# Kernel tuning notes

Hardware: AMD Instinct MI355X
Metric: run time of the kernel (lower is better)

## Reference

```python
import jax, jax.numpy as jnp
import numpy as np

B, T, DIN, P, HID, L = 256, 512, 25, 128, 256, 5
Q = 0.15
EPS = 1e-5


def setup_inputs() -> dict:
    key = jax.random.key(0)
    ks = jax.random.split(key, 12)
    s = 0.05
    return {
        "x": jax.random.normal(ks[0], (B, T, DIN), jnp.float32),
        "lengths": jax.random.randint(ks[1], (B,), 1, T + 1),
        "ln_g": jnp.ones((DIN,), jnp.float32),
        "ln_b": jnp.zeros((DIN,), jnp.float32),
        "w1": jax.random.normal(ks[2], (DIN, P), jnp.float32) * s,
        "b1": jnp.zeros((P,), jnp.float32),
        "w2": jax.random.normal(ks[3], (P, P), jnp.float32) * s,
        "b2": jnp.zeros((P,), jnp.float32),
        "Wih0": jax.random.normal(ks[4], (2, 3 * HID, P), jnp.float32) * s,
        "Whh0": jax.random.normal(ks[5], (2, 3 * HID, HID), jnp.float32) * s,
        "bih0": jnp.zeros((2, 3 * HID), jnp.float32),
        "bhh0": jnp.zeros((2, 3 * HID), jnp.float32),
        "Wih": jax.random.normal(ks[6], (L - 1, 2, 3 * HID, 2 * HID), jnp.float32) * s,
        "Whh": jax.random.normal(ks[7], (L - 1, 2, 3 * HID, HID), jnp.float32) * s,
        "bih": jnp.zeros((L - 1, 2, 3 * HID), jnp.float32),
        "bhh": jnp.zeros((L - 1, 2, 3 * HID), jnp.float32),
        "Wc": jax.random.normal(ks[8], (2 * HID,), jnp.float32) * s,
        "bc": jnp.zeros((), jnp.float32),
    }


def _gru_dir(xs, mask, Wih, Whh, bih, bhh):
    """Masked unidirectional GRU (PyTorch gate convention). xs:[B,T,Din], mask:[B,T] -> [B,T,HID]."""
    xw = jnp.einsum('btd,gd->btg', xs, Wih) + bih  # [B,T,3H] precomputed input gates

    def step(h, inp):
        xw_t, m_t = inp  # [B,3H], [B]
        gh = h @ Whh.T + bhh
        r = jax.nn.sigmoid(xw_t[:, :HID] + gh[:, :HID])
        z = jax.nn.sigmoid(xw_t[:, HID:2 * HID] + gh[:, HID:2 * HID])
        n = jnp.tanh(xw_t[:, 2 * HID:] + r * gh[:, 2 * HID:])
        h_new = (1.0 - z) * n + z * h
        h = jnp.where(m_t[:, None], h_new, h)        # hold state past sequence end (packing)
        return h, jnp.where(m_t[:, None], h, 0.0)    # padded outputs are zero (pad_packed)

    h0 = jnp.zeros((xs.shape[0], HID), xs.dtype)
    _, ys = jax.lax.scan(step, h0, (xw.transpose(1, 0, 2), mask.T))
    return ys.transpose(1, 0, 2)


def reference(x, lengths, ln_g, ln_b, w1, b1, w2, b2,
              Wih0, Whh0, bih0, bhh0, Wih, Whh, bih, bhh, Wc, bc):
    mask = jnp.arange(T)[None, :] < lengths[:, None]  # [B,T]

    # InputProjection: LayerNorm -> Linear -> GELU(exact) -> Linear
    mu = x.mean(-1, keepdims=True)
    var = ((x - mu) ** 2).mean(-1, keepdims=True)
    xn = (x - mu) / jnp.sqrt(var + EPS) * ln_g + ln_b
    h = jax.nn.gelu(xn @ w1 + b1, approximate=False) @ w2 + b2  # [B,T,P]

    # per-sample time reversal indices (reverse valid prefix only)
    rev = jnp.clip(lengths[:, None] - 1 - jnp.arange(T)[None, :], 0, T - 1)  # [B,T]

    inp = h
    for l in range(L):
        Wi = Wih0 if l == 0 else Wih[l - 1]
        Wh = Whh0 if l == 0 else Whh[l - 1]
        bi = bih0 if l == 0 else bih[l - 1]
        bh = bhh0 if l == 0 else bhh[l - 1]
        yf = _gru_dir(inp, mask, Wi[0], Wh[0], bi[0], bh[0])
        x_rev = jnp.take_along_axis(inp, rev[:, :, None], axis=1) * mask[:, :, None]
        yb_rev = _gru_dir(x_rev, mask, Wi[1], Wh[1], bi[1], bh[1])
        yb = jnp.take_along_axis(yb_rev, rev[:, :, None], axis=1) * mask[:, :, None]
        inp = jnp.concatenate([yf, yb], axis=-1)  # [B,T,2H]
    H = inp

    # TopQPooling: per-sample variable-k top-k by L2-norm score, then mean
    scores = jnp.where(mask, jnp.linalg.norm(H, axis=2), -1e9)
    k_vals = jnp.maximum(jnp.ceil(lengths.astype(jnp.float32) * Q).astype(jnp.int32), 1)  # [B]
    order = jnp.argsort(-scores, axis=1)                      # descending by score
    topmask = jnp.arange(T)[None, :] < k_vals[:, None]        # first k of sorted order
    Hs = jnp.take_along_axis(H, order[:, :, None], axis=1)
    pooled = (Hs * topmask[:, :, None]).sum(axis=1) / k_vals[:, None].astype(H.dtype)

    logits = pooled @ Wc + bc  # [B]
    return logits
```

## Files before the change

kernel.cpp:

```cpp
#include <hip/hip_runtime.h>
#include <math.h>


#define CH 64

__global__ __launch_bounds__(256)
void sort_k(const int* __restrict__ len, int* __restrict__ perm,
            int* __restrict__ nchp, int Bg)
{
    __shared__ int ll[256];
    __shared__ int lp[256];
    const int i = threadIdx.x;
    const int li = len[i];
    ll[i] = li;
    __syncthreads();
    int rk = 0;
    for (int j = 0; j < 256; j++) {
        int lj = ll[j];
        rk += (lj < li || (lj == li && j < i)) ? 1 : 0;
    }
    lp[rk] = i;
    __syncthreads();
    perm[i] = lp[i];
    const int ngrp = 256 / Bg;
    if (i < ngrp) {
        int mx = ll[lp[i * Bg + Bg - 1]];
        int nch = (mx + 63) >> 6;
        nchp[i] = nch < 1 ? 1 : (nch > 8 ? 8 : nch);
    }
}

__global__ __launch_bounds__(256)
void prep_whhT_k(const float* __restrict__ Whh0, const float* __restrict__ Whh,
                 float* __restrict__ out)
{
    int id = blockIdx.x * 256 + threadIdx.x;
    int u = id / 196608, rr = id % 196608;
    int k = rr / 768, c = rr % 768;
    int l = u >> 1, d = u & 1;
    out[id] = (l == 0) ? Whh0[(size_t)(d * 768 + c) * 256 + k]
                       : Whh[(size_t)(((l - 1) * 2 + d) * 768 + c) * 256 + k];
}

__global__ __launch_bounds__(128)
void input_proj_k(const float* __restrict__ x, const int* __restrict__ lengths,
                  const int* __restrict__ perm,
                  const float* __restrict__ lng, const float* __restrict__ lnb,
                  const float* __restrict__ w1, const float* __restrict__ b1v,
                  const float* __restrict__ w2, const float* __restrict__ b2v,
                  float* __restrict__ out, int g0)
{
    const int btl = blockIdx.x;
    const int sl  = btl >> 9;
    const int t   = btl & 511;
    const int b   = perm[g0 + sl];
    if (t >= lengths[b]) return;
    const int tid = threadIdx.x;
    __shared__ float xs[25];
    __shared__ float xn[25];
    __shared__ float hs[128];
    if (tid < 25) xs[tid] = x[((size_t)b * 512 + t) * 25 + tid];
    __syncthreads();
    if (tid < 25) {
        float mu = 0.f;
        #pragma unroll
        for (int k = 0; k < 25; k++) mu += xs[k];
        mu *= (1.f / 25.f);
        float var = 0.f;
        #pragma unroll
        for (int k = 0; k < 25; k++) { float dd = xs[k] - mu; var += dd * dd; }
        var *= (1.f / 25.f);
        float rstd = 1.f / sqrtf(var + 1e-5f);
        xn[tid] = (xs[tid] - mu) * rstd * lng[tid] + lnb[tid];
    }
    __syncthreads();
    float a = b1v[tid];
    #pragma unroll
    for (int k = 0; k < 25; k++) a = fmaf(xn[k], w1[k * 128 + tid], a);
    float ge = 0.5f * a * (1.f + erff(a * 0.70710678118654752440f));
    hs[tid] = ge;
    __syncthreads();
    float o = b2v[tid];
    #pragma unroll 8
    for (int k = 0; k < 128; k++) o = fmaf(hs[k], w2[k * 128 + tid], o);
    out[(size_t)btl * 128 + tid] = o;
}

__global__ __launch_bounds__(256)
void round_k(const float* __restrict__ A, int K,
             const float* __restrict__ W,
             const float* __restrict__ bi,
             const int* __restrict__ lengths, const int* __restrict__ perm,
             const int* __restrict__ nchp, int gidx, int g0, int Bg,
             float* __restrict__ xw_w,
             const float* __restrict__ xw_r,
             const float* __restrict__ whhT,
             const float* __restrict__ bhh,
             float* __restrict__ Y,
             float* __restrict__ hstate,
             int NR, int r)
{
    __shared__ float As[8][68];
    __shared__ float Bs[8][132];
    __shared__ float h_s[260];
    __shared__ float gs[4][776];

    const int tid = threadIdx.x;
    const int nch = nchp[gidx];

    if ((int)blockIdx.x < NR) {
        if (r == 0) return;
        const int d   = ((int)blockIdx.x >= Bg) ? 1 : 0;
        const int s   = (int)blockIdx.x - d * Bg;
        const int lo  = d ? (nch - r) * 64 : (r - 1) * 64;
        if (lo < 0 || lo >= 512) return;
        const int len = lengths[perm[g0 + s]];
        int nst = min(lo + CH, len) - lo;
        if (nst < 0) nst = 0;
        const int first = (r == 1);
        if (!first && nst <= 0) return;

        float* hg = hstate + (size_t)(d * Bg + s) * 256;
        h_s[tid] = first ? 0.f : hg[tid];
        __syncthreads();

        const int kq  = tid >> 6;
        const int q4  = (tid & 63) * 4;
        const float* Wd  = whhT + (size_t)d * 196608;
        const float* xwd = xw_r + (size_t)(d * Bg + s) * 64 * 768;
        const float bh0 = bhh[d * 768 + tid];
        const float bh1 = bhh[d * 768 + 256 + tid];
        const float bh2 = bhh[d * 768 + 512 + tid];

        for (int st = 0; st < nst; st++) {
            const int p = d ? (lo + nst - 1 - st) : (lo + st);
            float a0[4] = {}, a1[4] = {}, a2[4] = {};
            const float* wk = Wd + (size_t)(kq * 64) * 768 + q4;
            #pragma unroll 4
            for (int k4 = 0; k4 < 16; k4++) {
                float4 h4 = *(const float4*)&h_s[kq * 64 + k4 * 4];
                const float* w0 = wk + (size_t)(k4 * 4) * 768;
                float hk[4] = {h4.x, h4.y, h4.z, h4.w};
                #pragma unroll
                for (int kk = 0; kk < 4; kk++) {
                    const float* wr = w0 + (size_t)kk * 768;
                    float4 wv0 = *(const float4*)(wr);
                    float4 wv1 = *(const float4*)(wr + 256);
                    float4 wv2 = *(const float4*)(wr + 512);
                    float h = hk[kk];
                    a0[0] = fmaf(h, wv0.x, a0[0]); a0[1] = fmaf(h, wv0.y, a0[1]);
                    a0[2] = fmaf(h, wv0.z, a0[2]); a0[3] = fmaf(h, wv0.w, a0[3]);
                    a1[0] = fmaf(h, wv1.x, a1[0]); a1[1] = fmaf(h, wv1.y, a1[1]);
                    a1[2] = fmaf(h, wv1.z, a1[2]); a1[3] = fmaf(h, wv1.w, a1[3]);
                    a2[0] = fmaf(h, wv2.x, a2[0]); a2[1] = fmaf(h, wv2.y, a2[1]);
                    a2[2] = fmaf(h, wv2.z, a2[2]); a2[3] = fmaf(h, wv2.w, a2[3]);
                }
            }
            *(float4*)&gs[kq][q4]       = make_float4(a0[0], a0[1], a0[2], a0[3]);
            *(float4*)&gs[kq][256 + q4] = make_float4(a1[0], a1[1], a1[2], a1[3]);
            *(float4*)&gs[kq][512 + q4] = make_float4(a2[0], a2[1], a2[2], a2[3]);
            __syncthreads();
            float gr = bh0 + gs[0][tid] + gs[1][tid] + gs[2][tid] + gs[3][tid];
            float gz = bh1 + gs[0][256 + tid] + gs[1][256 + tid]
                           + gs[2][256 + tid] + gs[3][256 + tid];
            float gn = bh2 + gs[0][512 + tid] + gs[1][512 + tid]
                           + gs[2][512 + tid] + gs[3][512 + tid];
            const float* xr = xwd + (size_t)(p - lo) * 768;
            float rg = 1.f / (1.f + expf(-(xr[tid] + gr)));
            float zg = 1.f / (1.f + expf(-(xr[256 + tid] + gz)));
            float ng = tanhf(xr[512 + tid] + rg * gn);
            float hv = h_s[tid];
            float hn = (1.f - zg) * ng + zg * hv;
            h_s[tid] = hn;
            Y[((size_t)(s * 512 + p)) * 512 + d * 256 + tid] = hn;
            __syncthreads();
        }
        hg[tid] = h_s[tid];
    } else {
        const int gid  = blockIdx.x - NR;
        const int nt   = gid % 6;
        const int rest = gid / 6;
        const int d    = (rest >= Bg) ? 1 : 0;
        const int s    = rest - d * Bg;
        const int lo   = d ? (nch - 1 - r) * 64 : r * 64;
        if (lo < 0 || lo >= 512) return;
        if (lengths[perm[g0 + s]] <= lo) return;

        float acc[4][8] = {};
        const int tm = tid >> 4;
        const int tn = tid & 15;
        const int arr = tid >> 2, ak = (tid & 3) * 2;
        const int bn = tid >> 1, bk = (tid & 1) * 4;

        const float* Ap = A + (size_t)(s * 512 + lo + arr) * K + ak;
        const float* Wp = W + ((size_t)d * 768 + nt * 128 + bn) * K + bk;

        for (int k0 = 0; k0 < K; k0 += 8) {
            float2 av = *(const float2*)(Ap + k0);
            float4 bv = *(const float4*)(Wp + k0);
            __syncthreads();
            As[ak][arr] = av.x; As[ak + 1][arr] = av.y;
            Bs[bk + 0][bn] = bv.x; Bs[bk + 1][bn] = bv.y;
            Bs[bk + 2][bn] = bv.z; Bs[bk + 3][bn] = bv.w;
            __syncthreads();
            #pragma unroll
            for (int kk = 0; kk < 8; kk++) {
                float4 a4 = *(const float4*)&As[kk][tm * 4];
                float4 b0v = *(const float4*)&Bs[kk][tn * 4];
                float4 b1v = *(const float4*)&Bs[kk][64 + tn * 4];
                float ar4[4] = {a4.x, a4.y, a4.z, a4.w};
                float br[8] = {b0v.x, b0v.y, b0v.z, b0v.w,
                               b1v.x, b1v.y, b1v.z, b1v.w};
                #pragma unroll
                for (int i = 0; i < 4; i++)
                    #pragma unroll
                    for (int j = 0; j < 8; j++)
                        acc[i][j] = fmaf(ar4[i], br[j], acc[i][j]);
            }
        }
        const int cb = d * 768 + nt * 128;
        float bv0[4], bv1[4];
        #pragma unroll
        for (int j = 0; j < 4; j++) {
            bv0[j] = bi[cb + tn * 4 + j];
            bv1[j] = bi[cb + 64 + tn * 4 + j];
        }
        #pragma unroll
        for (int i = 0; i < 4; i++) {
            const int row = tm * 4 + i;
            float* o = xw_w + (size_t)((d * Bg + s) * 64 + row) * 768 + nt * 128 + tn * 4;
            float4 c0 = make_float4(acc[i][0] + bv0[0], acc[i][1] + bv0[1],
                                    acc[i][2] + bv0[2], acc[i][3] + bv0[3]);
            float4 c1 = make_float4(acc[i][4] + bv1[0], acc[i][5] + bv1[1],
                                    acc[i][6] + bv1[2], acc[i][7] + bv1[3]);
            *(float4*)(o)      = c0;
            *(float4*)(o + 64) = c1;
        }
    }
}

__global__ __launch_bounds__(256)
void pool_k(const float* __restrict__ H, const int* __restrict__ lengths,
            const int* __restrict__ perm,
            const float* __restrict__ Wc, const float* __restrict__ bcp,
            float* __restrict__ out, int g0)
{
    const int bl = blockIdx.x;
    const int b  = perm[g0 + bl];
    const int tid = threadIdx.x;
    __shared__ float sc[512];
    __shared__ int   sel[128];
    __shared__ int   nsel;
    __shared__ float red[256];
    const int len = lengths[b];
    const int k = max(1, (int)ceilf((float)len * 0.15f));
    if (tid == 0) nsel = 0;
    for (int t = tid; t < 512; t += 256) {
        float s;
        if (t < len) {
            const float* row = H + ((size_t)bl * 512 + t) * 512;
            float acc = 0.f;
            for (int j = 0; j < 512; j++) acc = fmaf(row[j], row[j], acc);
            s = sqrtf(acc);
        } else s = -1e9f;
        sc[t] = s;
    }
    __syncthreads();
    for (int t = tid; t < 512; t += 256) {
        if (t < len) {
            const float s = sc[t];
            int cnt = 0;
            for (int u = 0; u < 512; u++) {
                float su = sc[u];
                cnt += (su > s || (su == s && u < t)) ? 1 : 0;
            }
            if (cnt < k) { int p = atomicAdd(&nsel, 1); sel[p] = t; }
        }
    }
    __syncthreads();
    const int ns = nsel;
    float part = 0.f;
    for (int j = tid; j < 512; j += 256) {
        float acc = 0.f;
        for (int i = 0; i < ns; i++)
            acc += H[((size_t)bl * 512 + sel[i]) * 512 + j];
        part += (acc / (float)k) * Wc[j];
    }
    red[tid] = part;
    __syncthreads();
    for (int s2 = 128; s2 > 0; s2 >>= 1) {
        if (tid < s2) red[tid] += red[tid + s2];
        __syncthreads();
    }
    if (tid == 0) out[b] = red[0] + bcp[0];
}

static inline size_t alup(size_t x) { return (x + 255) & ~255ull; }

static size_t tier_bytes(int Bg)
{
    return 2 * alup((size_t)Bg * 512 * 512 * 4)
         + 2 * alup((size_t)Bg * 2 * 64 * 768 * 4)
         + alup(1966080ull * 4)
         + alup((size_t)Bg * 2 * 256 * 4)
         + alup(2048);
}

extern "C" void kernel_launch(void* const* d_in, const int* in_sizes, int n_in,
                              void* d_out, int out_size, void* d_ws, size_t ws_size,
                              hipStream_t stream)
{
    const float* x    = (const float*)d_in[0];
    const int*   len  = (const int*)  d_in[1];
    const float* ln_g = (const float*)d_in[2];
    const float* ln_b = (const float*)d_in[3];
    const float* w1   = (const float*)d_in[4];
    const float* b1   = (const float*)d_in[5];
    const float* w2   = (const float*)d_in[6];
    const float* b2   = (const float*)d_in[7];
    const float* Wih0 = (const float*)d_in[8];
    const float* Whh0 = (const float*)d_in[9];
    const float* bih0 = (const float*)d_in[10];
    const float* bhh0 = (const float*)d_in[11];
    const float* Wih  = (const float*)d_in[12];
    const float* Whh  = (const float*)d_in[13];
    const float* bih  = (const float*)d_in[14];
    const float* bhh  = (const float*)d_in[15];
    const float* Wc   = (const float*)d_in[16];
    const float* bc   = (const float*)d_in[17];
    float* out = (float*)d_out;

    int Bg = 0;
    const int tiers[5] = {128, 64, 32, 16, 8};
    for (int i = 0; i < 5; i++)
        if (ws_size >= tier_bytes(tiers[i])) { Bg = tiers[i]; break; }
    if (Bg == 0) return;

    char* ws = (char*)d_ws;
    size_t off = 0;
    auto alloc = [&](size_t bytes) { size_t o = off; off += alup(bytes); return o; };
    float* h0    = (float*)(ws + alloc((size_t)Bg * 512 * 512 * 4));
    float* h1    = (float*)(ws + alloc((size_t)Bg * 512 * 512 * 4));
    float* xwA   = (float*)(ws + alloc((size_t)Bg * 2 * 64 * 768 * 4));
    float* xwB   = (float*)(ws + alloc((size_t)Bg * 2 * 64 * 768 * 4));
    float* whhT  = (float*)(ws + alloc(1966080ull * 4));
    float* hst   = (float*)(ws + alloc((size_t)Bg * 2 * 256 * 4));
    int*   perm  = (int*)  (ws + alloc(2048));
    int*   nchp  = perm + 256;
    float* xwbuf[2] = {xwA, xwB};

    sort_k<<<1, 256, 0, stream>>>(len, perm, nchp, Bg);
    prep_whhT_k<<<7680, 256, 0, stream>>>(Whh0, Whh, whhT);

    const int NR = 2 * Bg;
    const int NG = 12 * Bg;

    for (int g0 = 0; g0 < 256; g0 += Bg) {
        const int gidx = g0 / Bg;
        input_proj_k<<<Bg * 512, 128, 0, stream>>>(x, len, perm, ln_g, ln_b,
                                                   w1, b1, w2, b2, h0, g0);
        float* bin = h0;
        float* bout = h1;
        for (int l = 0; l < 5; l++) {
            const int K = (l == 0) ? 128 : 512;
            const float* Wl  = (l == 0) ? Wih0 : (Wih + (size_t)(l - 1) * 2 * 768 * 512);
            const float* bil = (l == 0) ? bih0 : (bih + (size_t)(l - 1) * 1536);
            const float* whl = whhT + (size_t)l * 393216;
            const float* bhl = (l == 0) ? bhh0 : (bhh + (size_t)(l - 1) * 1536);
            for (int r = 0; r <= 8; r++) {
                round_k<<<NR + NG, 256, 0, stream>>>(
                    bin, K, Wl, bil, len, perm, nchp, gidx, g0, Bg,
                    xwbuf[r & 1], xwbuf[(r & 1) ^ 1],
                    whl, bhl, bout, hst, NR, r);
            }
            float* tmp = bin; bin = bout; bout = tmp;
        }
        pool_k<<<Bg, 256, 0, stream>>>(bin, len, perm, Wc, bc, out, g0);
    }
}
```

Measured before the change: 48.07 ms.

## Split GRU recurrence across 8-block groups with register-resident weights and flag sync

The recurrent part of each round is reorganised so that every block handles a 32-column slice of the hidden state for a group of 8 sequences, rather than one block computing the full 256-wide state of a single sequence. Each block keeps its slice of the recurrent weights in registers, so the Whh matrix is no longer re-streamed from memory at every timestep. After each step the blocks exchange hidden-state slices through a double-buffered global array, signalled with per-step release/acquire flags stamped with an epoch number. This spreads the serial matvec across more CUs and removes the repeated weight reads. In exchange it adds inter-block spin-waiting, relies on all 8 blocks of a group being co-resident to avoid deadlock, and processes padded steps up to the longest length in each group.

```diff
diff --git a/kernel.cpp b/kernel.cpp
--- a/kernel.cpp
+++ b/kernel.cpp
@@ -3,6 +3,11 @@
 
 
 #define CH 64
+
+#define AT_LOAD_RLX(p)    __hip_atomic_load((p),  __ATOMIC_RELAXED, __HIP_MEMORY_SCOPE_AGENT)
+#define AT_LOAD_ACQ(p)    __hip_atomic_load((p),  __ATOMIC_ACQUIRE, __HIP_MEMORY_SCOPE_AGENT)
+#define AT_STORE_RLX(p,v) __hip_atomic_store((p),(v),__ATOMIC_RELAXED, __HIP_MEMORY_SCOPE_AGENT)
+#define AT_STORE_REL(p,v) __hip_atomic_store((p),(v),__ATOMIC_RELEASE, __HIP_MEMORY_SCOPE_AGENT)
 
 __global__ __launch_bounds__(256)
 void sort_k(const int* __restrict__ len, int* __restrict__ perm,
@@ -97,13 +102,14 @@
              const float* __restrict__ whhT,
              const float* __restrict__ bhh,
              float* __restrict__ Y,
-             float* __restrict__ hstate,
-             int NR, int r)
+             int* __restrict__ hx,
+             int* __restrict__ flags,
+             int NR, int r, int epoch)
 {
     __shared__ float As[8][68];
     __shared__ float Bs[8][132];
-    __shared__ float h_s[260];
-    __shared__ float gs[4][776];
+    __shared__ float hsh[8][256];
+    __shared__ float gsb[8][8][96];
 
     const int tid = threadIdx.x;
     const int nch = nchp[gidx];
@@ -111,71 +117,124 @@
     if ((int)blockIdx.x < NR) {
         if (r == 0) return;
         const int d   = ((int)blockIdx.x >= Bg) ? 1 : 0;
-        const int s   = (int)blockIdx.x - d * Bg;
-        const int lo  = d ? (nch - r) * 64 : (r - 1) * 64;
+        const int rr2 = (int)blockIdx.x - d * Bg;
+        const int sg  = rr2 >> 3;
+        const int sl  = rr2 & 7;
+        const int lo  = d ? (nch - r) * CH : (r - 1) * CH;
         if (lo < 0 || lo >= 512) return;
-        const int len = lengths[perm[g0 + s]];
-        int nst = min(lo + CH, len) - lo;
-        if (nst < 0) nst = 0;
-        const int first = (r == 1);
-        if (!first && nst <= 0) return;
-
-        float* hg = hstate + (size_t)(d * Bg + s) * 256;
-        h_s[tid] = first ? 0.f : hg[tid];
+        const int mlsg = lengths[perm[g0 + sg * 8 + 7]];
+        int nst = min(lo + CH, mlsg) - lo;
+        if (nst <= 0) return;
+        const bool first = d ? (mlsg <= lo + CH) : (r == 1);
+
+        const int kq = tid >> 5;
+        const int jj = tid & 31;
+
+        const float* wb = whhT + (size_t)d * 196608 + (size_t)(kq * 32) * 768
+                        + sl * 32 + jj;
+        float w0[32], w1[32], w2[32];
+        #pragma unroll
+        for (int k = 0; k < 32; k++) {
+            const float* wr = wb + (size_t)k * 768;
+            w0[k] = wr[0];
+            w1[k] = wr[256];
+            w2[k] = wr[512];
+        }
+
+        const int s2 = tid >> 5;
+        const int j2 = tid & 31;
+        const int lens2 = lengths[perm[g0 + sg * 8 + s2]];
+        const float bh0 = bhh[d * 768 +       sl * 32 + j2];
+        const float bh1 = bhh[d * 768 + 256 + sl * 32 + j2];
+        const float bh2 = bhh[d * 768 + 512 + sl * 32 + j2];
+        const int sgN = Bg >> 3;
+        int* flg = flags + (size_t)((d * sgN + sg) * 8) * 64;
+        const int PS  = 2 * Bg * 256;
+        const int hxq = (d * Bg + sg * 8) * 256;
+        float* hf = &hsh[0][0];
+
+        if (first) {
+            #pragma unroll
+            for (int i = 0; i < 8; i++) hf[tid * 8 + i] = 0.f;
+        } else {
+            const int pprev = d ? (lo + nst) : (lo - 1);
+            const int par0  = pprev & 1;
+            #pragma unroll
+            for (int i = 0; i < 8; i++) {
+                const int m = tid * 8 + i;
+                hf[m] = __int_as_float(AT_LOAD_RLX(&hx[par0 * PS + hxq + m]));
+            }
+        }
         __syncthreads();
 
-        const int kq  = tid >> 6;
-        const int q4  = (tid & 63) * 4;
-        const float* Wd  = whhT + (size_t)d * 196608;
-        const float* xwd = xw_r + (size_t)(d * Bg + s) * 64 * 768;
-        const float bh0 = bhh[d * 768 + tid];
-        const float bh1 = bhh[d * 768 + 256 + tid];
-        const float bh2 = bhh[d * 768 + 512 + tid];
+        const float* xwd = xw_r + (size_t)(d * Bg + sg * 8) * 64 * 768 + sl * 32 + j2;
+        const int m0   = tid * 8;
+        const int dim0 = m0 & 255;
+        int* fpoll = &flg[(dim0 >> 5) * 64];
 
         for (int st = 0; st < nst; st++) {
-            const int p = d ? (lo + nst - 1 - st) : (lo + st);
-            float a0[4] = {}, a1[4] = {}, a2[4] = {};
-            const float* wk = Wd + (size_t)(kq * 64) * 768 + q4;
-            #pragma unroll 4
-            for (int k4 = 0; k4 < 16; k4++) {
-                float4 h4 = *(const float4*)&h_s[kq * 64 + k4 * 4];
-                const float* w0 = wk + (size_t)(k4 * 4) * 768;
-                float hk[4] = {h4.x, h4.y, h4.z, h4.w};
+            const int p   = d ? (lo + nst - 1 - st) : (lo + st);
+            const int row = p - lo;
+            const float* xr = xwd + (size_t)(s2 * 64 + row) * 768;
+            const float xv0 = xr[0], xv1 = xr[256], xv2 = xr[512];
+
+            #pragma unroll
+            for (int s = 0; s < 8; s++) {
+                float b0 = 0.f, b1 = 0.f, b2 = 0.f;
                 #pragma unroll
-                for (int kk = 0; kk < 4; kk++) {
-                    const float* wr = w0 + (size_t)kk * 768;
-                    float4 wv0 = *(const float4*)(wr);
-                    float4 wv1 = *(const float4*)(wr + 256);
-                    float4 wv2 = *(const float4*)(wr + 512);
-                    float h = hk[kk];
-                    a0[0] = fmaf(h, wv0.x, a0[0]); a0[1] = fmaf(h, wv0.y, a0[1]);
-                    a0[2] = fmaf(h, wv0.z, a0[2]); a0[3] = fmaf(h, wv0.w, a0[3]);
-                    a1[0] = fmaf(h, wv1.x, a1[0]); a1[1] = fmaf(h, wv1.y, a1[1]);
-                    a1[2] = fmaf(h, wv1.z, a1[2]); a1[3] = fmaf(h, wv1.w, a1[3]);
-                    a2[0] = fmaf(h, wv2.x, a2[0]); a2[1] = fmaf(h, wv2.y, a2[1]);
-                    a2[2] = fmaf(h, wv2.z, a2[2]); a2[3] = fmaf(h, wv2.w, a2[3]);
+                for (int k4 = 0; k4 < 8; k4++) {
+                    const float4 h4 = *(const float4*)&hsh[s][kq * 32 + k4 * 4];
+                    b0 = fmaf(h4.x, w0[k4 * 4 + 0], b0);
+                    b0 = fmaf(h4.y, w0[k4 * 4 + 1], b0);
+                    b0 = fmaf(h4.z, w0[k4 * 4 + 2], b0);
+                    b0 = fmaf(h4.w, w0[k4 * 4 + 3], b0);
+                    b1 = fmaf(h4.x, w1[k4 * 4 + 0], b1);
+                    b1 = fmaf(h4.y, w1[k4 * 4 + 1], b1);
+                    b1 = fmaf(h4.z, w1[k4 * 4 + 2], b1);
+                    b1 = fmaf(h4.w, w1[k4 * 4 + 3], b1);
+                    b2 = fmaf(h4.x, w2[k4 * 4 + 0], b2);
+                    b2 = fmaf(h4.y, w2[k4 * 4 + 1], b2);
+                    b2 = fmaf(h4.z, w2[k4 * 4 + 2], b2);
+                    b2 = fmaf(h4.w, w2[k4 * 4 + 3], b2);
                 }
-            }
-            *(float4*)&gs[kq][q4]       = make_float4(a0[0], a0[1], a0[2], a0[3]);
-            *(float4*)&gs[kq][256 + q4] = make_float4(a1[0], a1[1], a1[2], a1[3]);
-            *(float4*)&gs[kq][512 + q4] = make_float4(a2[0], a2[1], a2[2], a2[3]);
+                gsb[kq][s][jj]      = b0;
+                gsb[kq][s][32 + jj] = b1;
+                gsb[kq][s][64 + jj] = b2;
+            }
             __syncthreads();
-            float gr = bh0 + gs[0][tid] + gs[1][tid] + gs[2][tid] + gs[3][tid];
-            float gz = bh1 + gs[0][256 + tid] + gs[1][256 + tid]
-                           + gs[2][256 + tid] + gs[3][256 + tid];
-            float gn = bh2 + gs[0][512 + tid] + gs[1][512 + tid]
-                           + gs[2][512 + tid] + gs[3][512 + tid];
-            const float* xr = xwd + (size_t)(p - lo) * 768;
-            float rg = 1.f / (1.f + expf(-(xr[tid] + gr)));
-            float zg = 1.f / (1.f + expf(-(xr[256 + tid] + gz)));
-            float ng = tanhf(xr[512 + tid] + rg * gn);
-            float hv = h_s[tid];
+
+            float gr = bh0, gz = bh1, gn = bh2;
+            #pragma unroll
+            for (int q = 0; q < 8; q++) {
+                gr += gsb[q][s2][j2];
+                gz += gsb[q][s2][32 + j2];
+                gn += gsb[q][s2][64 + j2];
+            }
+            const float rg = 1.f / (1.f + expf(-(xv0 + gr)));
+            const float zg = 1.f / (1.f + expf(-(xv1 + gz)));
+            const float ng = tanhf(xv2 + rg * gn);
+            const float hv = hsh[s2][sl * 32 + j2];
             float hn = (1.f - zg) * ng + zg * hv;
-            h_s[tid] = hn;
-            Y[((size_t)(s * 512 + p)) * 512 + d * 256 + tid] = hn;
+            if (p >= lens2) hn = hv;
+            const int par = p & 1;
+            AT_STORE_RLX(&hx[par * PS + hxq + s2 * 256 + sl * 32 + j2],
+                         __float_as_int(hn));
+            if (p < lens2)
+                Y[((size_t)((sg * 8 + s2) * 512 + p)) * 512 + d * 256 + sl * 32 + j2] = hn;
             __syncthreads();
-        }
-        hg[tid] = h_s[tid];
+
+            if (st == nst - 1) break;
+            if (tid == 0) AT_STORE_REL(&flg[sl * 64 + st], epoch);
+            {
+                int* f = fpoll + st;
+                while (AT_LOAD_ACQ(f) != epoch) __builtin_amdgcn_s_sleep(2);
+                #pragma unroll
+                for (int i = 0; i < 8; i++)
+                    hf[m0 + i] = __int_as_float(
+                        AT_LOAD_RLX(&hx[par * PS + hxq + m0 + i]));
+            }
+            __syncthreads();
+        }
     } else {
         const int gid  = blockIdx.x - NR;
         const int nt   = gid % 6;
@@ -302,7 +361,8 @@
     return 2 * alup((size_t)Bg * 512 * 512 * 4)
          + 2 * alup((size_t)Bg * 2 * 64 * 768 * 4)
          + alup(1966080ull * 4)
-         + alup((size_t)Bg * 2 * 256 * 4)
+         + alup((size_t)4 * Bg * 256 * 4)
+         + alup((size_t)2 * (Bg / 8) * 8 * 64 * 4)
          + alup(2048);
 }
 
@@ -344,10 +404,14 @@
     float* xwA   = (float*)(ws + alloc((size_t)Bg * 2 * 64 * 768 * 4));
     float* xwB   = (float*)(ws + alloc((size_t)Bg * 2 * 64 * 768 * 4));
     float* whhT  = (float*)(ws + alloc(1966080ull * 4));
-    float* hst   = (float*)(ws + alloc((size_t)Bg * 2 * 256 * 4));
+    int*   hx    = (int*)  (ws + alloc((size_t)4 * Bg * 256 * 4));
+    const size_t flagBytes = (size_t)2 * (Bg / 8) * 8 * 64 * 4;
+    int*   flags = (int*)  (ws + alloc(flagBytes));
     int*   perm  = (int*)  (ws + alloc(2048));
     int*   nchp  = perm + 256;
     float* xwbuf[2] = {xwA, xwB};
+
+    hipMemsetAsync(flags, 0, flagBytes, stream);
 
     sort_k<<<1, 256, 0, stream>>>(len, perm, nchp, Bg);
     prep_whhT_k<<<7680, 256, 0, stream>>>(Whh0, Whh, whhT);
@@ -368,10 +432,11 @@
             const float* whl = whhT + (size_t)l * 393216;
             const float* bhl = (l == 0) ? bhh0 : (bhh + (size_t)(l - 1) * 1536);
             for (int r = 0; r <= 8; r++) {
+                const int ep = (gidx * 5 + l) * 9 + r + 1;
                 round_k<<<NR + NG, 256, 0, stream>>>(
                     bin, K, Wl, bil, len, perm, nchp, gidx, g0, Bg,
                     xwbuf[r & 1], xwbuf[(r & 1) ^ 1],
-                    whl, bhl, bout, hst, NR, r);
+                    whl, bhl, bout, hx, flags, NR, r, ep);
             }
             float* tmp = bin; bin = bout; bout = tmp;
         }
```

After: 78.57 ms. 63.4% more time.

## Batch eight sequences per recurrent block to reuse Whh loads across samples

Applied to the files above, without the earlier changes.

The recurrent GRU blocks now each process eight length-sorted sequences together instead of one. Each thread owns one hidden unit across all three gates and reads Whh once per step, reusing it for eight hidden states. This replaces the split-K shared-memory reduction, removes one barrier per step, and double-buffers h. The Whh transpose layout changes to match, padded steps are masked per sample, and a Bg=256 workspace tier is added. The trade-off is fewer recurrent blocks (NR = Bg/4), so less parallelism on the serial critical path, with more registers per thread.

```diff
diff --git a/kernel.cpp b/kernel.cpp
--- a/kernel.cpp
+++ b/kernel.cpp
@@ -35,11 +35,15 @@
                  float* __restrict__ out)
 {
     int id = blockIdx.x * 256 + threadIdx.x;
-    int u = id / 196608, rr = id % 196608;
-    int k = rr / 768, c = rr % 768;
-    int l = u >> 1, d = u & 1;
-    out[id] = (l == 0) ? Whh0[(size_t)(d * 768 + c) * 256 + k]
-                       : Whh[(size_t)(((l - 1) * 2 + d) * 768 + c) * 256 + k];
+    int kp = id & 3;  int rest = id >> 2;
+    int j  = rest & 255; rest >>= 8;
+    int g3 = rest % 3;   rest /= 3;
+    int k4 = rest & 63;  rest >>= 6;
+    int l = rest >> 1, d = rest & 1;
+    int row = g3 * 256 + j;
+    int col = k4 * 4 + kp;
+    out[id] = (l == 0) ? Whh0[(size_t)(d * 768 + row) * 256 + col]
+                       : Whh[(size_t)(((l - 1) * 2 + d) * 768 + row) * 256 + col];
 }
 
 __global__ __launch_bounds__(128)
@@ -100,83 +104,102 @@
              float* __restrict__ hstate,
              int NR, int r)
 {
-    __shared__ float As[8][68];
-    __shared__ float Bs[8][132];
-    __shared__ float h_s[260];
-    __shared__ float gs[4][776];
+    __shared__ float smem[4096];
 
     const int tid = threadIdx.x;
     const int nch = nchp[gidx];
 
     if ((int)blockIdx.x < NR) {
         if (r == 0) return;
-        const int d   = ((int)blockIdx.x >= Bg) ? 1 : 0;
-        const int s   = (int)blockIdx.x - d * Bg;
-        const int lo  = d ? (nch - r) * 64 : (r - 1) * 64;
+        const int half = NR >> 1;
+        const int d  = ((int)blockIdx.x >= half) ? 1 : 0;
+        const int sg = (int)blockIdx.x - d * half;
+        const int lo = d ? (nch - r) * CH : (r - 1) * CH;
         if (lo < 0 || lo >= 512) return;
-        const int len = lengths[perm[g0 + s]];
-        int nst = min(lo + CH, len) - lo;
-        if (nst < 0) nst = 0;
-        const int first = (r == 1);
-        if (!first && nst <= 0) return;
-
-        float* hg = hstate + (size_t)(d * Bg + s) * 256;
-        h_s[tid] = first ? 0.f : hg[tid];
-        __syncthreads();
-
-        const int kq  = tid >> 6;
-        const int q4  = (tid & 63) * 4;
-        const float* Wd  = whhT + (size_t)d * 196608;
-        const float* xwd = xw_r + (size_t)(d * Bg + s) * 64 * 768;
+        const int mlsg = lengths[perm[g0 + sg * 8 + 7]];
+        int nst = min(lo + CH, mlsg) - lo;
+        if (nst <= 0) return;
+        const bool first = d ? (mlsg <= lo + CH) : (r == 1);
+
+        float* h_cur = smem;
+        float* h_nxt = smem + 2048;
+
+        int lenv[8];
+        #pragma unroll
+        for (int s = 0; s < 8; s++) lenv[s] = lengths[perm[g0 + sg * 8 + s]];
+
         const float bh0 = bhh[d * 768 + tid];
         const float bh1 = bhh[d * 768 + 256 + tid];
         const float bh2 = bhh[d * 768 + 512 + tid];
 
+        float* hst = hstate + (size_t)(d * Bg + sg * 8) * 256;
+        if (first) {
+            #pragma unroll
+            for (int s = 0; s < 8; s++) h_cur[s * 256 + tid] = 0.f;
+        } else {
+            #pragma unroll
+            for (int s = 0; s < 8; s++) h_cur[s * 256 + tid] = hst[s * 256 + tid];
+        }
+        __syncthreads();
+
+        const float4* wd4 = (const float4*)whhT + (size_t)d * 49152 + tid;
+        const float* xb = xw_r + ((size_t)(d * Bg + sg * 8) * 64) * 768 + tid;
+
         for (int st = 0; st < nst; st++) {
-            const int p = d ? (lo + nst - 1 - st) : (lo + st);
-            float a0[4] = {}, a1[4] = {}, a2[4] = {};
-            const float* wk = Wd + (size_t)(kq * 64) * 768 + q4;
-            #pragma unroll 4
-            for (int k4 = 0; k4 < 16; k4++) {
-                float4 h4 = *(const float4*)&h_s[kq * 64 + k4 * 4];
-                const float* w0 = wk + (size_t)(k4 * 4) * 768;
-                float hk[4] = {h4.x, h4.y, h4.z, h4.w};
+            const int p   = d ? (lo + nst - 1 - st) : (lo + st);
+            const int row = p - lo;
+
+            float a0[8], a1[8], a2[8];
+            #pragma unroll
+            for (int s = 0; s < 8; s++) { a0[s] = 0.f; a1[s] = 0.f; a2[s] = 0.f; }
+
+            #pragma unroll 8
+            for (int k4 = 0; k4 < 64; k4++) {
+                const float4 w0v = wd4[(k4 * 3 + 0) * 256];
+                const float4 w1v = wd4[(k4 * 3 + 1) * 256];
+                const float4 w2v = wd4[(k4 * 3 + 2) * 256];
                 #pragma unroll
-                for (int kk = 0; kk < 4; kk++) {
-                    const float* wr = w0 + (size_t)kk * 768;
-                    float4 wv0 = *(const float4*)(wr);
-                    float4 wv1 = *(const float4*)(wr + 256);
-                    float4 wv2 = *(const float4*)(wr + 512);
-                    float h = hk[kk];
-                    a0[0] = fmaf(h, wv0.x, a0[0]); a0[1] = fmaf(h, wv0.y, a0[1]);
-                    a0[2] = fmaf(h, wv0.z, a0[2]); a0[3] = fmaf(h, wv0.w, a0[3]);
-                    a1[0] = fmaf(h, wv1.x, a1[0]); a1[1] = fmaf(h, wv1.y, a1[1]);
-                    a1[2] = fmaf(h, wv1.z, a1[2]); a1[3] = fmaf(h, wv1.w, a1[3]);
-                    a2[0] = fmaf(h, wv2.x, a2[0]); a2[1] = fmaf(h, wv2.y, a2[1]);
-                    a2[2] = fmaf(h, wv2.z, a2[2]); a2[3] = fmaf(h, wv2.w, a2[3]);
+                for (int s = 0; s < 8; s++) {
+                    const float4 h4 = *(const float4*)&h_cur[s * 256 + k4 * 4];
+                    a0[s] = fmaf(h4.x, w0v.x, a0[s]);
+                    a0[s] = fmaf(h4.y, w0v.y, a0[s]);
+                    a0[s] = fmaf(h4.z, w0v.z, a0[s]);
+                    a0[s] = fmaf(h4.w, w0v.w, a0[s]);
+                    a1[s] = fmaf(h4.x, w1v.x, a1[s]);
+                    a1[s] = fmaf(h4.y, w1v.y, a1[s]);
+                    a1[s] = fmaf(h4.z, w1v.z, a1[s]);
+                    a1[s] = fmaf(h4.w, w1v.w, a1[s]);
+                    a2[s] = fmaf(h4.x, w2v.x, a2[s]);
+                    a2[s] = fmaf(h4.y, w2v.y, a2[s]);
+                    a2[s] = fmaf(h4.z, w2v.z, a2[s]);
+                    a2[s] = fmaf(h4.w, w2v.w, a2[s]);
                 }
             }
-            *(float4*)&gs[kq][q4]       = make_float4(a0[0], a0[1], a0[2], a0[3]);
-            *(float4*)&gs[kq][256 + q4] = make_float4(a1[0], a1[1], a1[2], a1[3]);
-            *(float4*)&gs[kq][512 + q4] = make_float4(a2[0], a2[1], a2[2], a2[3]);
+
+            const float* xr0 = xb + (size_t)row * 768;
+            #pragma unroll
+            for (int s = 0; s < 8; s++) {
+                const float* xr = xr0 + (size_t)s * 49152;
+                const float xv0 = xr[0], xv1 = xr[256], xv2 = xr[512];
+                const float rg = 1.f / (1.f + expf(-(xv0 + a0[s] + bh0)));
+                const float zg = 1.f / (1.f + expf(-(xv1 + a1[s] + bh1)));
+                const float ng = tanhf(xv2 + rg * (a2[s] + bh2));
+                const float hv = h_cur[s * 256 + tid];
+                float hn = (1.f - zg) * ng + zg * hv;
+                if (p >= lenv[s]) hn = hv;
+                h_nxt[s * 256 + tid] = hn;
+                if (p < lenv[s])
+                    Y[((size_t)((sg * 8 + s) * 512 + p)) * 512 + d * 256 + tid] = hn;
+            }
             __syncthreads();
-            float gr = bh0 + gs[0][tid] + gs[1][tid] + gs[2][tid] + gs[3][tid];
-            float gz = bh1 + gs[0][256 + tid] + gs[1][256 + tid]
-                           + gs[2][256 + tid] + gs[3][256 + tid];
-            float gn = bh2 + gs[0][512 + tid] + gs[1][512 + tid]
-                           + gs[2][512 + tid] + gs[3][512 + tid];
-            const float* xr = xwd + (size_t)(p - lo) * 768;
-            float rg = 1.f / (1.f + expf(-(xr[tid] + gr)));
-            float zg = 1.f / (1.f + expf(-(xr[256 + tid] + gz)));
-            float ng = tanhf(xr[512 + tid] + rg * gn);
-            float hv = h_s[tid];
-            float hn = (1.f - zg) * ng + zg * hv;
-            h_s[tid] = hn;
-            Y[((size_t)(s * 512 + p)) * 512 + d * 256 + tid] = hn;
-            __syncthreads();
-        }
-        hg[tid] = h_s[tid];
+            float* t = h_cur; h_cur = h_nxt; h_nxt = t;
+        }
+        #pragma unroll
+        for (int s = 0; s < 8; s++) hst[s * 256 + tid] = h_cur[s * 256 + tid];
     } else {
+        float (*As)[68]  = (float(*)[68])smem;
+        float (*Bs)[132] = (float(*)[132])(smem + 544);
+
         const int gid  = blockIdx.x - NR;
         const int nt   = gid % 6;
         const int rest = gid / 6;
@@ -302,7 +325,7 @@
     return 2 * alup((size_t)Bg * 512 * 512 * 4)
          + 2 * alup((size_t)Bg * 2 * 64 * 768 * 4)
          + alup(1966080ull * 4)
-         + alup((size_t)Bg * 2 * 256 * 4)
+         + alup((size_t)2 * Bg * 256 * 4)
          + alup(2048);
 }
 
@@ -331,8 +354,8 @@
     float* out = (float*)d_out;
 
     int Bg = 0;
-    const int tiers[5] = {128, 64, 32, 16, 8};
-    for (int i = 0; i < 5; i++)
+    const int tiers[6] = {256, 128, 64, 32, 16, 8};
+    for (int i = 0; i < 6; i++)
         if (ws_size >= tier_bytes(tiers[i])) { Bg = tiers[i]; break; }
     if (Bg == 0) return;
 
@@ -344,7 +367,7 @@
     float* xwA   = (float*)(ws + alloc((size_t)Bg * 2 * 64 * 768 * 4));
     float* xwB   = (float*)(ws + alloc((size_t)Bg * 2 * 64 * 768 * 4));
     float* whhT  = (float*)(ws + alloc(1966080ull * 4));
-    float* hst   = (float*)(ws + alloc((size_t)Bg * 2 * 256 * 4));
+    float* hst   = (float*)(ws + alloc((size_t)2 * Bg * 256 * 4));
     int*   perm  = (int*)  (ws + alloc(2048));
     int*   nchp  = perm + 256;
     float* xwbuf[2] = {xwA, xwB};
@@ -352,7 +375,7 @@
     sort_k<<<1, 256, 0, stream>>>(len, perm, nchp, Bg);
     prep_whhT_k<<<7680, 256, 0, stream>>>(Whh0, Whh, whhT);
 
-    const int NR = 2 * Bg;
+    const int NR = Bg >> 2;
     const int NG = 12 * Bg;
 
     for (int g0 = 0; g0 < 256; g0 += Bg) {
```

After: 186.5 ms. 3.88x slower.

## Process two sequences per recurrent block to share Whh loads

Applied to the files above, without the earlier changes.

Each recurrent block now advances two length-sorted sequences together, so every Whh weight load is reused for two hidden-state FMAs. This halves the number of recurrent blocks and the weight traffic per step. Per-sequence masking keeps the shorter sequence's state and outputs correct, and the block runs until the longer one ends. Shared memory is merged into one union buffer, and a 256-sequence group tier is added so larger workspaces need fewer passes. The costs are higher register pressure from doubled accumulators and wasted steps when paired lengths differ.

```diff
diff --git a/kernel.cpp b/kernel.cpp
--- a/kernel.cpp
+++ b/kernel.cpp
@@ -100,83 +100,123 @@
              float* __restrict__ hstate,
              int NR, int r)
 {
-    __shared__ float As[8][68];
-    __shared__ float Bs[8][132];
-    __shared__ float h_s[260];
-    __shared__ float gs[4][776];
+    __shared__ float smem[6728];
 
     const int tid = threadIdx.x;
     const int nch = nchp[gidx];
 
     if ((int)blockIdx.x < NR) {
         if (r == 0) return;
-        const int d   = ((int)blockIdx.x >= Bg) ? 1 : 0;
-        const int s   = (int)blockIdx.x - d * Bg;
-        const int lo  = d ? (nch - r) * 64 : (r - 1) * 64;
+        const int half = NR >> 1;
+        const int d  = ((int)blockIdx.x >= half) ? 1 : 0;
+        const int pg = (int)blockIdx.x - d * half;
+        const int s0 = pg * 2;
+        const int lo = d ? (nch - r) * CH : (r - 1) * CH;
         if (lo < 0 || lo >= 512) return;
-        const int len = lengths[perm[g0 + s]];
-        int nst = min(lo + CH, len) - lo;
-        if (nst < 0) nst = 0;
-        const int first = (r == 1);
-        if (!first && nst <= 0) return;
-
-        float* hg = hstate + (size_t)(d * Bg + s) * 256;
-        h_s[tid] = first ? 0.f : hg[tid];
+        const int len0 = lengths[perm[g0 + s0]];
+        const int len1 = lengths[perm[g0 + s0 + 1]];
+        int nst = min(lo + CH, len1) - lo;
+        if (nst <= 0) return;
+        const bool first = d ? (len1 <= lo + CH) : (r == 1);
+
+        float* h_s0 = smem;
+        float* h_s1 = smem + 260;
+        float* gs   = smem + 520;
+
+        float* hg = hstate + (size_t)(d * Bg + s0) * 256;
+        if (first) {
+            h_s0[tid] = 0.f;
+            h_s1[tid] = 0.f;
+        } else {
+            h_s0[tid] = hg[tid];
+            h_s1[tid] = hg[256 + tid];
+        }
         __syncthreads();
 
         const int kq  = tid >> 6;
         const int q4  = (tid & 63) * 4;
         const float* Wd  = whhT + (size_t)d * 196608;
-        const float* xwd = xw_r + (size_t)(d * Bg + s) * 64 * 768;
+        const float* xw0 = xw_r + (size_t)(d * Bg + s0) * 64 * 768;
+        const float* xw1 = xw0 + 49152;
         const float bh0 = bhh[d * 768 + tid];
         const float bh1 = bhh[d * 768 + 256 + tid];
         const float bh2 = bhh[d * 768 + 512 + tid];
 
         for (int st = 0; st < nst; st++) {
-            const int p = d ? (lo + nst - 1 - st) : (lo + st);
-            float a0[4] = {}, a1[4] = {}, a2[4] = {};
+            const int p   = d ? (lo + nst - 1 - st) : (lo + st);
+            const int row = p - lo;
+            float a0a[4] = {}, a1a[4] = {}, a2a[4] = {};
+            float a0b[4] = {}, a1b[4] = {}, a2b[4] = {};
             const float* wk = Wd + (size_t)(kq * 64) * 768 + q4;
             #pragma unroll 4
             for (int k4 = 0; k4 < 16; k4++) {
-                float4 h4 = *(const float4*)&h_s[kq * 64 + k4 * 4];
+                float4 h4a = *(const float4*)&h_s0[kq * 64 + k4 * 4];
+                float4 h4b = *(const float4*)&h_s1[kq * 64 + k4 * 4];
                 const float* w0 = wk + (size_t)(k4 * 4) * 768;
-                float hk[4] = {h4.x, h4.y, h4.z, h4.w};
+                float ha[4] = {h4a.x, h4a.y, h4a.z, h4a.w};
+                float hb[4] = {h4b.x, h4b.y, h4b.z, h4b.w};
                 #pragma unroll
                 for (int kk = 0; kk < 4; kk++) {
                     const float* wr = w0 + (size_t)kk * 768;
                     float4 wv0 = *(const float4*)(wr);
                     float4 wv1 = *(const float4*)(wr + 256);
                     float4 wv2 = *(const float4*)(wr + 512);
-                    float h = hk[kk];
-                    a0[0] = fmaf(h, wv0.x, a0[0]); a0[1] = fmaf(h, wv0.y, a0[1]);
-                    a0[2] = fmaf(h, wv0.z, a0[2]); a0[3] = fmaf(h, wv0.w, a0[3]);
-                    a1[0] = fmaf(h, wv1.x, a1[0]); a1[1] = fmaf(h, wv1.y, a1[1]);
-                    a1[2] = fmaf(h, wv1.z, a1[2]); a1[3] = fmaf(h, wv1.w, a1[3]);
-                    a2[0] = fmaf(h, wv2.x, a2[0]); a2[1] = fmaf(h, wv2.y, a2[1]);
-                    a2[2] = fmaf(h, wv2.z, a2[2]); a2[3] = fmaf(h, wv2.w, a2[3]);
+                    float hav = ha[kk], hbv = hb[kk];
+                    a0a[0] = fmaf(hav, wv0.x, a0a[0]); a0a[1] = fmaf(hav, wv0.y, a0a[1]);
+                    a0a[2] = fmaf(hav, wv0.z, a0a[2]); a0a[3] = fmaf(hav, wv0.w, a0a[3]);
+                    a1a[0] = fmaf(hav, wv1.x, a1a[0]); a1a[1] = fmaf(hav, wv1.y, a1a[1]);
+                    a1a[2] = fmaf(hav, wv1.z, a1a[2]); a1a[3] = fmaf(hav, wv1.w, a1a[3]);
+                    a2a[0] = fmaf(hav, wv2.x, a2a[0]); a2a[1] = fmaf(hav, wv2.y, a2a[1]);
+                    a2a[2] = fmaf(hav, wv2.z, a2a[2]); a2a[3] = fmaf(hav, wv2.w, a2a[3]);
+                    a0b[0] = fmaf(hbv, wv0.x, a0b[0]); a0b[1] = fmaf(hbv, wv0.y, a0b[1]);
+                    a0b[2] = fmaf(hbv, wv0.z, a0b[2]); a0b[3] = fmaf(hbv, wv0.w, a0b[3]);
+                    a1b[0] = fmaf(hbv, wv1.x, a1b[0]); a1b[1] = fmaf(hbv, wv1.y, a1b[1]);
+                    a1b[2] = fmaf(hbv, wv1.z, a1b[2]); a1b[3] = fmaf(hbv, wv1.w, a1b[3]);
+                    a2b[0] = fmaf(hbv, wv2.x, a2b[0]); a2b[1] = fmaf(hbv, wv2.y, a2b[1]);
+                    a2b[2] = fmaf(hbv, wv2.z, a2b[2]); a2b[3] = fmaf(hbv, wv2.w, a2b[3]);
                 }
             }
-            *(float4*)&gs[kq][q4]       = make_float4(a0[0], a0[1], a0[2], a0[3]);
-            *(float4*)&gs[kq][256 + q4] = make_float4(a1[0], a1[1], a1[2], a1[3]);
-            *(float4*)&gs[kq][512 + q4] = make_float4(a2[0], a2[1], a2[2], a2[3]);
+            {
+                float* g0p = gs + (size_t)kq * 776;
+                float* g1p = gs + (size_t)(4 + kq) * 776;
+                *(float4*)&g0p[q4]       = make_float4(a0a[0], a0a[1], a0a[2], a0a[3]);
+                *(float4*)&g0p[256 + q4] = make_float4(a1a[0], a1a[1], a1a[2], a1a[3]);
+                *(float4*)&g0p[512 + q4] = make_float4(a2a[0], a2a[1], a2a[2], a2a[3]);
+                *(float4*)&g1p[q4]       = make_float4(a0b[0], a0b[1], a0b[2], a0b[3]);
+                *(float4*)&g1p[256 + q4] = make_float4(a1b[0], a1b[1], a1b[2], a1b[3]);
+                *(float4*)&g1p[512 + q4] = make_float4(a2b[0], a2b[1], a2b[2], a2b[3]);
+            }
             __syncthreads();
-            float gr = bh0 + gs[0][tid] + gs[1][tid] + gs[2][tid] + gs[3][tid];
-            float gz = bh1 + gs[0][256 + tid] + gs[1][256 + tid]
-                           + gs[2][256 + tid] + gs[3][256 + tid];
-            float gn = bh2 + gs[0][512 + tid] + gs[1][512 + tid]
-                           + gs[2][512 + tid] + gs[3][512 + tid];
-            const float* xr = xwd + (size_t)(p - lo) * 768;
-            float rg = 1.f / (1.f + expf(-(xr[tid] + gr)));
-            float zg = 1.f / (1.f + expf(-(xr[256 + tid] + gz)));
-            float ng = tanhf(xr[512 + tid] + rg * gn);
-            float hv = h_s[tid];
-            float hn = (1.f - zg) * ng + zg * hv;
-            h_s[tid] = hn;
-            Y[((size_t)(s * 512 + p)) * 512 + d * 256 + tid] = hn;
+            #pragma unroll
+            for (int sp = 0; sp < 2; sp++) {
+                const float* gp = gs + (size_t)(sp * 4) * 776;
+                float gr = bh0 + gp[tid] + gp[776 + tid]
+                               + gp[1552 + tid] + gp[2328 + tid];
+                float gz = bh1 + gp[256 + tid] + gp[1032 + tid]
+                               + gp[1808 + tid] + gp[2584 + tid];
+                float gn = bh2 + gp[512 + tid] + gp[1288 + tid]
+                               + gp[2064 + tid] + gp[2840 + tid];
+                const float* xr = (sp ? xw1 : xw0) + (size_t)row * 768;
+                float rg = 1.f / (1.f + expf(-(xr[tid] + gr)));
+                float zg = 1.f / (1.f + expf(-(xr[256 + tid] + gz)));
+                float ng = tanhf(xr[512 + tid] + rg * gn);
+                float* hsp = sp ? h_s1 : h_s0;
+                const int lensp = sp ? len1 : len0;
+                float hv = hsp[tid];
+                float hn = (1.f - zg) * ng + zg * hv;
+                if (p >= lensp) hn = hv;
+                hsp[tid] = hn;
+                if (p < lensp)
+                    Y[((size_t)((s0 + sp) * 512 + p)) * 512 + d * 256 + tid] = hn;
+            }
             __syncthreads();
         }
-        hg[tid] = h_s[tid];
+        hg[tid]       = h_s0[tid];
+        hg[256 + tid] = h_s1[tid];
     } else {
+        float (*As)[68]  = (float(*)[68])smem;
+        float (*Bs)[132] = (float(*)[132])(smem + 544);
+
         const int gid  = blockIdx.x - NR;
         const int nt   = gid % 6;
         const int rest = gid / 6;
@@ -302,7 +342,7 @@
     return 2 * alup((size_t)Bg * 512 * 512 * 4)
          + 2 * alup((size_t)Bg * 2 * 64 * 768 * 4)
          + alup(1966080ull * 4)
-         + alup((size_t)Bg * 2 * 256 * 4)
+         + alup((size_t)2 * Bg * 256 * 4)
          + alup(2048);
 }
 
@@ -331,8 +371,8 @@
     float* out = (float*)d_out;
 
     int Bg = 0;
-    const int tiers[5] = {128, 64, 32, 16, 8};
-    for (int i = 0; i < 5; i++)
+    const int tiers[6] = {256, 128, 64, 32, 16, 8};
+    for (int i = 0; i < 6; i++)
         if (ws_size >= tier_bytes(tiers[i])) { Bg = tiers[i]; break; }
     if (Bg == 0) return;
 
@@ -344,7 +384,7 @@
     float* xwA   = (float*)(ws + alloc((size_t)Bg * 2 * 64 * 768 * 4));
     float* xwB   = (float*)(ws + alloc((size_t)Bg * 2 * 64 * 768 * 4));
     float* whhT  = (float*)(ws + alloc(1966080ull * 4));
-    float* hst   = (float*)(ws + alloc((size_t)Bg * 2 * 256 * 4));
+    float* hst   = (float*)(ws + alloc((size_t)2 * Bg * 256 * 4));
     int*   perm  = (int*)  (ws + alloc(2048));
     int*   nchp  = perm + 256;
     float* xwbuf[2] = {xwA, xwB};
@@ -352,7 +392,7 @@
     sort_k<<<1, 256, 0, stream>>>(len, perm, nchp, Bg);
     prep_whhT_k<<<7680, 256, 0, stream>>>(Whh0, Whh, whhT);
 
-    const int NR = 2 * Bg;
+    const int NR = Bg;
     const int NG = 12 * Bg;
 
     for (int g0 = 0; g0 < 256; g0 += Bg) {
```

Measured after the change: 56.71 ms. +18.0%, slower.
